# Kernel tuning notes

Measured on AMD Instinct MI355X. Metric: run time of the kernel, lower is better.

Reference implementation:

```python
import jax, jax.numpy as jnp
import numpy as np

B, T, E = 4, 2048, 2048
NH, NKV, HD = 16, 4, 128
THETA = 10000.0


def _rope(x, pos_ids, theta):
    # x: [b, h, t, hd]; pos_ids: [b, t]; theta: [hd/2]
    ang = pos_ids[:, None, :, None].astype(jnp.float32) * theta  # [b,1,t,hd/2]
    cos, sin = jnp.cos(ang), jnp.sin(ang)
    x1, x2 = x[..., ::2], x[..., 1::2]
    # interleave rotated pairs back to [..., hd]
    rot = jnp.stack([x1 * cos - x2 * sin, x1 * sin + x2 * cos], axis=-1)
    return rot.reshape(x.shape)


def setup_inputs() -> dict:
    key = jax.random.key(0)
    ks = jax.random.split(key, 10)
    s = 0.02
    x = jax.random.normal(ks[0], (B, T, E), dtype=jnp.float32)
    attention_mask = jax.random.randint(ks[1], (B, T, T), 0, 2, dtype=jnp.int32)
    # torch nn.Linear weights stored here as [in, out] (y = x @ W + b)
    Wq = jax.random.normal(ks[2], (E, E), dtype=jnp.float32) * s
    bq = jnp.zeros((E,), dtype=jnp.float32)
    Wk = jax.random.normal(ks[3], (E, NKV * HD), dtype=jnp.float32) * s
    bk = jnp.zeros((NKV * HD,), dtype=jnp.float32)
    Wv = jax.random.normal(ks[4], (E, NKV * HD), dtype=jnp.float32) * s
    bv = jnp.zeros((NKV * HD,), dtype=jnp.float32)
    Wo = jax.random.normal(ks[5], (E, E), dtype=jnp.float32) * s
    bo = jnp.zeros((E,), dtype=jnp.float32)
    return {"x": x, "attention_mask": attention_mask, "Wq": Wq, "bq": bq,
            "Wk": Wk, "bk": bk, "Wv": Wv, "bv": bv, "Wo": Wo, "bo": bo}


def reference(x, attention_mask, Wq, bq, Wk, bk, Wv, bv, Wo, bo):
    b, t = x.shape[0], x.shape[1]
    # faithful to original: plain reshape (view), NOT transpose-based head split
    q = (x @ Wq + bq).reshape(b, NH, t, HD)
    k = (x @ Wk + bk).reshape(b, NKV, t, HD)
    v = (x @ Wv + bv).reshape(b, NKV, t, HD)
    theta = THETA ** (-jnp.arange(0, HD, 2, dtype=jnp.float32) / HD)
    pos = jnp.broadcast_to(jnp.arange(t), (b, t))
    # original RoPE.forward is wrapped in @torch.no_grad() -> stop_gradient
    k = jax.lax.stop_gradient(_rope(k, pos, theta))
    v = jax.lax.stop_gradient(_rope(v, pos, theta))  # note: RoPE applied to V too
    g = NH // NKV
    k = jnp.tile(k, (1, g, 1, 1))  # torch .repeat tiles kv heads
    v = jnp.tile(v, (1, g, 1, 1))
    # original divides by head_dim ** (-0.5) == multiply by sqrt(head_dim)
    scores = jnp.einsum('bhqd,bhkd->bhqk', q, k) * (HD ** 0.5)
    scores = jnp.where(attention_mask[:, None, :, :] == 0, jnp.float32(1e-9), scores)
    attn = jax.nn.softmax(scores, axis=-1)  # dropout inactive (eval mode)
    out = jnp.einsum('bhqk,bhkd->bhqd', attn, v)
    out = out.transpose(0, 2, 1, 3).reshape(b, t, NH * HD)
    return out @ Wo + bo
```

## Files before the change

### kernel.cpp

```cpp
#include <hip/hip_runtime.h>
#include <math.h>

constexpr int Bc   = 4;
constexpr int Tc   = 2048;
constexpr int Ec   = 2048;
constexpr int NHc  = 16;
constexpr int NKVc = 4;
constexpr int HDc  = 128;
constexpr int KVEc = NKVc * HDc;

typedef __attribute__((ext_vector_type(8))) short bf16x8;
typedef __attribute__((ext_vector_type(4))) short short4v;
typedef __attribute__((ext_vector_type(4))) float f32x4;

__device__ __forceinline__ short f2bf(float f) {
    union { float f; unsigned u; } v; v.f = f;
    unsigned r = v.u + 0x7FFF + ((v.u >> 16) & 1);
    return (short)(r >> 16);
}
__device__ __forceinline__ float bf2f(short s) {
    union { unsigned u; float f; } v; v.u = ((unsigned)(unsigned short)s) << 16;
    return v.f;
}
__device__ __forceinline__ float ex2(float x) {
    float r; asm("v_exp_f32 %0, %1" : "=v"(r) : "v"(x)); return r;
}
__device__ __forceinline__ void gload16(const void* g, void* l) {
    __builtin_amdgcn_global_load_lds(
        (const __attribute__((address_space(1))) unsigned*)g,
        (__attribute__((address_space(3))) unsigned*)l, 16, 0, 0);
}

__global__ __launch_bounds__(256)
void convert_split(const float* __restrict__ X, short* __restrict__ Xhi,
                   short* __restrict__ Xlo)
{
    int i = blockIdx.x * 256 + threadIdx.x;
    float4 v = ((const float4*)X)[i];
    float fv[4] = {v.x, v.y, v.z, v.w};
    short4v hi, lo;
    #pragma unroll
    for (int j = 0; j < 4; ++j) {
        hi[j] = f2bf(fv[j]);
        lo[j] = f2bf(fv[j] - bf2f(hi[j]));
    }
    ((short4v*)Xhi)[i] = hi;
    ((short4v*)Xlo)[i] = lo;
}

__global__ __launch_bounds__(256)
void transpose_split(const float* __restrict__ W, short* __restrict__ WThi,
                     short* __restrict__ WTlo, int K, int N)
{
    __shared__ float Ls[32][33];
    const int k0 = blockIdx.x * 32, n0 = blockIdx.y * 32;
    const int t = threadIdx.x;
    const int r = t >> 3, c4 = (t & 7) << 2;
    float4 v = *(const float4*)(W + (size_t)(k0 + r) * N + n0 + c4);
    Ls[r][c4 + 0] = v.x; Ls[r][c4 + 1] = v.y;
    Ls[r][c4 + 2] = v.z; Ls[r][c4 + 3] = v.w;
    __syncthreads();
    short4v hi, lo;
    #pragma unroll
    for (int i = 0; i < 4; ++i) {
        float f = Ls[c4 + i][r];
        hi[i] = f2bf(f);
        lo[i] = f2bf(f - bf2f(hi[i]));
    }
    *(short4v*)(WThi + (size_t)(n0 + r) * K + k0 + c4) = hi;
    if (WTlo) *(short4v*)(WTlo + (size_t)(n0 + r) * K + k0 + c4) = lo;
}

__global__ __launch_bounds__(256)
void mask_bits(const int* __restrict__ mask, unsigned long long* __restrict__ Mb)
{
    const int widx = blockIdx.x * 4 + (threadIdx.x >> 6);
    const int L = threadIdx.x & 63;
    const int m = mask[(size_t)widx * 64 + L];
    unsigned long long bits = __ballot(m != 0);
    if (L == 0) Mb[widx] = bits;
}

template <bool SPLIT>
__global__ __launch_bounds__(256, 2)
void gemm_mfma(const short* __restrict__ Ahi, const short* __restrict__ Alo,
               const short* __restrict__ Bhi, const short* __restrict__ Blo,
               const float* __restrict__ bias, float* __restrict__ C,
               int M, int N, int K)
{
    __shared__ short AsH[128 * 32];
    __shared__ short BsH[128 * 32];
    __shared__ short AsL[SPLIT ? 128 * 32 : 8];
    __shared__ short BsL[SPLIT ? 128 * 32 : 8];

    const int t = threadIdx.x;
    const int w = t >> 6, L = t & 63;
    const int l16 = L & 15, quad = L >> 4;
    const int wr = w >> 1, wc = w & 1;
    const int bm = blockIdx.x * 128, bn = blockIdx.y * 128;

    const int sm = L >> 2;
    const int sq = ((L & 3) - (sm >> 2)) & 3;
    const int scol = sq * 8;

    f32x4 acc[4][4];
    #pragma unroll
    for (int mi = 0; mi < 4; ++mi)
        #pragma unroll
        for (int ni = 0; ni < 4; ++ni) acc[mi][ni] = (f32x4){0, 0, 0, 0};

    const int fxor = (quad + (l16 >> 2)) & 3;

    for (int k0 = 0; k0 < K; k0 += 32) {
        __syncthreads();
        #pragma unroll
        for (int i = 0; i < 2; ++i) {
            const int wl = w * 2 + i;
            const size_t ra = (size_t)(bm + wl * 16 + sm) * K + k0 + scol;
            const size_t rb = (size_t)(bn + wl * 16 + sm) * K + k0 + scol;
            gload16(Ahi + ra, &AsH[wl * 512]);
            gload16(Bhi + rb, &BsH[wl * 512]);
            if (SPLIT) {
                gload16(Alo + ra, &AsL[wl * 512]);
                gload16(Blo + rb, &BsL[wl * 512]);
            }
        }
        __syncthreads();

        bf16x8 ah[4], bh[4], al[4], bl[4];
        #pragma unroll
        for (int mi = 0; mi < 4; ++mi) {
            const int ch = ((wr * 4 + mi) * 64 + l16 * 4 + fxor) * 8;
            ah[mi] = *(const bf16x8*)&AsH[ch];
            if (SPLIT) al[mi] = *(const bf16x8*)&AsL[ch];
        }
        #pragma unroll
        for (int ni = 0; ni < 4; ++ni) {
            const int ch = ((wc * 4 + ni) * 64 + l16 * 4 + fxor) * 8;
            bh[ni] = *(const bf16x8*)&BsH[ch];
            if (SPLIT) bl[ni] = *(const bf16x8*)&BsL[ch];
        }
        #pragma unroll
        for (int mi = 0; mi < 4; ++mi)
            #pragma unroll
            for (int ni = 0; ni < 4; ++ni) {
                acc[mi][ni] = __builtin_amdgcn_mfma_f32_16x16x32_bf16(
                    ah[mi], bh[ni], acc[mi][ni], 0, 0, 0);
                if (SPLIT) {
                    acc[mi][ni] = __builtin_amdgcn_mfma_f32_16x16x32_bf16(
                        al[mi], bh[ni], acc[mi][ni], 0, 0, 0);
                    acc[mi][ni] = __builtin_amdgcn_mfma_f32_16x16x32_bf16(
                        ah[mi], bl[ni], acc[mi][ni], 0, 0, 0);
                }
            }
    }

    #pragma unroll
    for (int ni = 0; ni < 4; ++ni) {
        const int col = bn + wc * 64 + ni * 16 + l16;
        const float bv = bias[col];
        #pragma unroll
        for (int mi = 0; mi < 4; ++mi) {
            #pragma unroll
            for (int r = 0; r < 4; ++r) {
                const int row = bm + wr * 64 + mi * 16 + quad * 4 + r;
                C[(size_t)row * N + col] = acc[mi][ni][r] + bv;
            }
        }
    }
}

__global__ __launch_bounds__(256)
void rope_k(const float* __restrict__ X2d, short* __restrict__ Khi,
            short* __restrict__ Klo)
{
    const int idx = blockIdx.x * 256 + threadIdx.x;
    const int j  = idx & 63;
    const int tk = (idx >> 6) & (Tc - 1);
    const int kh = (idx >> 17) & (NKVc - 1);
    const int bb = idx >> 19;
    const int row = (kh << 9) + (tk >> 2);
    const int col = ((tk & 3) << 7) + (j << 1);
    const float* src = X2d + ((size_t)bb * Tc + row) * KVEc + col;
    const float a = src[0];
    const float b = src[1];
    const float theta = powf(10000.0f, -(float)j * (1.0f / 64.0f));
    const float ang = (float)tk * theta;
    float s, c;
    sincosf(ang, &s, &c);
    const float r0 = a * c - b * s;
    const float r1 = a * s + b * c;
    const size_t off = (((size_t)bb * NKVc + kh) * Tc + tk) * HDc + (j << 1);
    short h0 = f2bf(r0), h1 = f2bf(r1);
    Khi[off]     = h0;  Klo[off]     = f2bf(r0 - bf2f(h0));
    Khi[off + 1] = h1;  Klo[off + 1] = f2bf(r1 - bf2f(h1));
}

__global__ __launch_bounds__(256)
void rope_v_t(const float* __restrict__ V2d, short* __restrict__ Vt)
{
    __shared__ short Ls[128][40];
    const int g  = blockIdx.x;
    const int kh = blockIdx.y;
    const int bb = blockIdx.z;
    const int t  = threadIdx.x;

    const float* src = V2d + ((size_t)bb * Tc + (kh << 9) + (g << 3)) * KVEc;
    #pragma unroll
    for (int i = 0; i < 4; ++i) {
        int e = i * 256 + t;
        float4 v = ((const float4*)src)[e];
        int row = e >> 7;
        int col = (e & 127) << 2;
        int tkl = (row << 2) + (col >> 7);
        int d0  = col & 127;
        int tk  = (g << 5) + tkl;
        float fv[4] = {v.x, v.y, v.z, v.w};
        #pragma unroll
        for (int p = 0; p < 2; ++p) {
            int j = (d0 >> 1) + p;
            float theta = powf(10000.0f, -(float)j * (1.0f / 64.0f));
            float ang = (float)tk * theta;
            float s, c;
            sincosf(ang, &s, &c);
            float a = fv[2 * p], b = fv[2 * p + 1];
            Ls[d0 + 2 * p    ][tkl] = f2bf(a * c - b * s);
            Ls[d0 + 2 * p + 1][tkl] = f2bf(a * s + b * c);
        }
    }
    __syncthreads();
    const int d = t >> 1;
    const int h16 = (t & 1) << 4;
    short* dst = Vt + (((size_t)bb * NKVc + kh) * HDc + d) * Tc + (g << 5) + h16;
    bf16x8 o0 = *(const bf16x8*)&Ls[d][h16];
    bf16x8 o1 = *(const bf16x8*)&Ls[d][h16 + 8];
    *(bf16x8*)dst = o0;
    *(bf16x8*)(dst + 8) = o1;
}

__global__ __launch_bounds__(256, 3)
void attn_mfma(const float* __restrict__ Q2d, const short* __restrict__ Khi_g,
               const short* __restrict__ Klo_g, const short* __restrict__ Vt_g,
               const unsigned long long* __restrict__ Mb, short* __restrict__ AObf)
{
    __shared__ short KhiS[64 * 128];
    __shared__ short KloS[64 * 128];
    __shared__ short VtS [128 * 64];

    const int fid  = blockIdx.x + 32 * (blockIdx.y + 16 * blockIdx.z);
    const int slot = fid >> 3;
    const int grp  = (fid & 7) + 8 * (slot >> 5);
    const int qb   = slot & 31;
    const int h    = grp & 15;
    const int bb   = grp >> 4;

    const int t    = threadIdx.x;
    const int w    = t >> 6;
    const int L    = t & 63;
    const int l16  = L & 15;
    const int quad = L >> 4;
    const int q1v  = quad >> 1;
    const int kh   = h & (NKVc - 1);
    const int tq0  = qb * 64 + w * 16;

    bf16x8 qhi[4], qlo[4];
    {
        const float* qrow = Q2d +
            ((size_t)(bb * Tc + h * HDc + qb * 4 + w)) * Ec + 128 * l16;
        #pragma unroll
        for (int kc = 0; kc < 4; ++kc) {
            const float* p = qrow + kc * 32 + quad * 8;
            #pragma unroll
            for (int j = 0; j < 8; ++j) {
                float f = p[j];
                short hi = f2bf(f);
                qhi[kc][j] = hi;
                qlo[kc][j] = f2bf(f - bf2f(hi));
            }
        }
    }

    float m_r = -INFINITY, lp = 0.0f;
    f32x4 o[8];
    #pragma unroll
    for (int nc = 0; nc < 8; ++nc) o[nc] = (f32x4){0, 0, 0, 0};

    const short* kbh = Khi_g + ((size_t)(bb * NKVc + kh)) * Tc * HDc;
    const short* kbl = Klo_g + ((size_t)(bb * NKVc + kh)) * Tc * HDc;
    const short* vb  = Vt_g  + ((size_t)(bb * NKVc + kh)) * HDc * Tc;
    const unsigned long long* mrow =
        Mb + ((size_t)(bb * Tc + tq0 + l16)) * (Tc / 64);

    constexpr float SCALE2  = 11.313708498984761f * 1.4426950408889634f;
    constexpr float MASKED2 = 1e-9f * 1.4426950408889634f;

    const int km   = L >> 4;
    const int kpos = L & 15;
    const int vm   = L >> 3;
    const int vc   = ((L & 7) - vm) & 7;

    const int srcA = l16 + 16 * ((2 * quad)     & 3);
    const int srcB = l16 + 16 * ((2 * quad + 1) & 3);

    auto stageK = [&](int kt) {
        #pragma unroll
        for (int i = 0; i < 4; ++i) {
            const int wl = w * 4 + i;
            const int krow = wl * 4 + km;
            const int kc_ = (kpos - (krow & 15)) & 15;
            const size_t go = (size_t)(kt * 64 + krow) * HDc + kc_ * 8;
            gload16(kbh + go, &KhiS[wl * 512]);
            gload16(kbl + go, &KloS[wl * 512]);
        }
    };
    auto stageV = [&](int kt) {
        #pragma unroll
        for (int i = 0; i < 4; ++i) {
            const int wl = w * 4 + i;
            const int vrow = wl * 8 + vm;
            gload16(vb + (size_t)vrow * Tc + kt * 64 + vc * 8, &VtS[wl * 512]);
        }
    };

    asm volatile("s_waitcnt vmcnt(0)" ::: "memory");
    stageK(0);
    __builtin_amdgcn_sched_barrier(0);
    stageV(0);
    unsigned long long mw = mrow[0];

    for (int kt = 0; kt < Tc / 64; ++kt) {
        const int ktn = (kt + 1) & 31;

        asm volatile("s_waitcnt vmcnt(5)" ::: "memory");
        __builtin_amdgcn_s_barrier();
        __builtin_amdgcn_sched_barrier(0);

        f32x4 s[4];
        #pragma unroll
        for (int nt = 0; nt < 4; ++nt) {
            f32x4 acc = (f32x4){0, 0, 0, 0};
            #pragma unroll
            for (int kc = 0; kc < 4; ++kc) {
                const int ch = (((nt * 4 + (l16 >> 2)) << 6) + ((l16 & 3) << 4)
                                + ((kc * 4 + quad + l16) & 15)) << 3;
                bf16x8 khiF = *(const bf16x8*)&KhiS[ch];
                bf16x8 kloF = *(const bf16x8*)&KloS[ch];
                acc = __builtin_amdgcn_mfma_f32_16x16x32_bf16(khiF, qhi[kc], acc, 0, 0, 0);
                acc = __builtin_amdgcn_mfma_f32_16x16x32_bf16(khiF, qlo[kc], acc, 0, 0, 0);
                acc = __builtin_amdgcn_mfma_f32_16x16x32_bf16(kloF, qhi[kc], acc, 0, 0, 0);
            }
            s[nt] = acc;
        }

        asm volatile("s_waitcnt lgkmcnt(0)" ::: "memory");
        __builtin_amdgcn_sched_barrier(0);
        __builtin_amdgcn_s_barrier();
        __builtin_amdgcn_sched_barrier(0);
        stageK(ktn);
        __builtin_amdgcn_sched_barrier(0);

        const unsigned mlo = (unsigned)mw;
        const unsigned mhi = (unsigned)(mw >> 32);
        const int gq = quad << 2;
        const unsigned fm[4] = { mlo >> gq, (mlo >> 16) >> gq,
                                 mhi >> gq, (mhi >> 16) >> gq };
        #pragma unroll
        for (int nt = 0; nt < 4; ++nt)
            #pragma unroll
            for (int r = 0; r < 4; ++r)
                s[nt][r] = (fm[nt] & (1u << r)) ? s[nt][r] * SCALE2 : MASKED2;

        float mt;
        {
            float a0 = fmaxf(fmaxf(s[0][0], s[0][1]), fmaxf(s[0][2], s[0][3]));
            float a1 = fmaxf(fmaxf(s[1][0], s[1][1]), fmaxf(s[1][2], s[1][3]));
            float a2 = fmaxf(fmaxf(s[2][0], s[2][1]), fmaxf(s[2][2], s[2][3]));
            float a3 = fmaxf(fmaxf(s[3][0], s[3][1]), fmaxf(s[3][2], s[3][3]));
            mt = fmaxf(fmaxf(a0, a1), fmaxf(a2, a3));
        }
        mt = fmaxf(mt, __shfl_xor(mt, 16));
        mt = fmaxf(mt, __shfl_xor(mt, 32));

        const bool res = (mt > m_r + 8.0f);
        if (__any(res)) {
            const float mn_ = res ? mt : m_r;
            const float alq = ex2(m_r - mn_);
            m_r = mn_;
            lp *= alq;
            float alo[4];
            #pragma unroll
            for (int r = 0; r < 4; ++r)
                alo[r] = __shfl(alq, quad * 16 + quad * 4 + r);
            #pragma unroll
            for (int nc = 0; nc < 8; ++nc)
                #pragma unroll
                for (int r = 0; r < 4; ++r)
                    o[nc][r] *= alo[r];
        }

        float rs;
        {
            float t0 = 0.f, t1 = 0.f;
            #pragma unroll
            for (int nt = 0; nt < 4; ++nt) {
                float p0 = ex2(s[nt][0] - m_r);
                float p1 = ex2(s[nt][1] - m_r);
                float p2 = ex2(s[nt][2] - m_r);
                float p3 = ex2(s[nt][3] - m_r);
                s[nt][0] = p0; s[nt][1] = p1; s[nt][2] = p2; s[nt][3] = p3;
                t0 += p0 + p1; t1 += p2 + p3;
            }
            rs = t0 + t1;
        }
        lp += rs;

        int pk00, pk01, pk10, pk11, pk20, pk21, pk30, pk31;
        asm("v_cvt_pk_bf16_f32 %0, %1, %2" : "=v"(pk00) : "v"(s[0][0]), "v"(s[0][1]));
        asm("v_cvt_pk_bf16_f32 %0, %1, %2" : "=v"(pk01) : "v"(s[0][2]), "v"(s[0][3]));
        asm("v_cvt_pk_bf16_f32 %0, %1, %2" : "=v"(pk10) : "v"(s[1][0]), "v"(s[1][1]));
        asm("v_cvt_pk_bf16_f32 %0, %1, %2" : "=v"(pk11) : "v"(s[1][2]), "v"(s[1][3]));
        asm("v_cvt_pk_bf16_f32 %0, %1, %2" : "=v"(pk20) : "v"(s[2][0]), "v"(s[2][1]));
        asm("v_cvt_pk_bf16_f32 %0, %1, %2" : "=v"(pk21) : "v"(s[2][2]), "v"(s[2][3]));
        asm("v_cvt_pk_bf16_f32 %0, %1, %2" : "=v"(pk30) : "v"(s[3][0]), "v"(s[3][1]));
        asm("v_cvt_pk_bf16_f32 %0, %1, %2" : "=v"(pk31) : "v"(s[3][2]), "v"(s[3][3]));

        union U { int d[4]; bf16x8 v; } A0, A1;
        {
            int u0, u1;
            u0 = __shfl(pk00, srcA); u1 = __shfl(pk10, srcA); A0.d[0] = q1v ? u1 : u0;
            u0 = __shfl(pk01, srcA); u1 = __shfl(pk11, srcA); A0.d[1] = q1v ? u1 : u0;
            u0 = __shfl(pk00, srcB); u1 = __shfl(pk10, srcB); A0.d[2] = q1v ? u1 : u0;
            u0 = __shfl(pk01, srcB); u1 = __shfl(pk11, srcB); A0.d[3] = q1v ? u1 : u0;
            u0 = __shfl(pk20, srcA); u1 = __shfl(pk30, srcA); A1.d[0] = q1v ? u1 : u0;
            u0 = __shfl(pk21, srcA); u1 = __shfl(pk31, srcA); A1.d[1] = q1v ? u1 : u0;
            u0 = __shfl(pk20, srcB); u1 = __shfl(pk30, srcB); A1.d[2] = q1v ? u1 : u0;
            u0 = __shfl(pk21, srcB); u1 = __shfl(pk31, srcB); A1.d[3] = q1v ? u1 : u0;
        }

        asm volatile("s_waitcnt vmcnt(8)" ::: "memory");
        __builtin_amdgcn_s_barrier();
        __builtin_amdgcn_sched_barrier(0);

        #pragma unroll
        for (int nc = 0; nc < 8; ++nc) {
            const int rg = (nc * 2 + (l16 >> 3)) << 6;
            const int rm = l16 & 7;
            const int ch0 = (rg + (rm << 3) + ((quad + rm) & 7)) << 3;
            const int ch1 = (rg + (rm << 3) + ((quad + 4 + rm) & 7)) << 3;
            bf16x8 b0 = *(const bf16x8*)&VtS[ch0];
            bf16x8 b1 = *(const bf16x8*)&VtS[ch1];
            o[nc] = __builtin_amdgcn_mfma_f32_16x16x32_bf16(A0.v, b0, o[nc], 0, 0, 0);
            o[nc] = __builtin_amdgcn_mfma_f32_16x16x32_bf16(A1.v, b1, o[nc], 0, 0, 0);
        }

        asm volatile("s_waitcnt lgkmcnt(0)" ::: "memory");
        __builtin_amdgcn_sched_barrier(0);
        __builtin_amdgcn_s_barrier();
        __builtin_amdgcn_sched_barrier(0);
        stageV(ktn);
        mw = mrow[ktn];
    }

    asm volatile("s_waitcnt vmcnt(0)" ::: "memory");

    lp += __shfl_xor(lp, 16);
    lp += __shfl_xor(lp, 32);
    const float invl = 1.0f / lp;
    float invo[4];
    #pragma unroll
    for (int r = 0; r < 4; ++r)
        invo[r] = __shfl(invl, quad * 16 + quad * 4 + r);

    #pragma unroll
    for (int r = 0; r < 4; ++r) {
        short* orow = AObf + ((size_t)(bb * Tc + tq0 + quad * 4 + r)) * Ec
                           + h * HDc + l16;
        #pragma unroll
        for (int nc = 0; nc < 8; ++nc)
            orow[nc * 16] = f2bf(o[nc][r] * invo[r]);
    }
}

extern "C" void kernel_launch(void* const* d_in, const int* in_sizes, int n_in,
                              void* d_out, int out_size, void* d_ws, size_t ws_size,
                              hipStream_t stream)
{
    const float* x    = (const float*)d_in[0];
    const int*  amask = (const int*)  d_in[1];
    const float* Wq   = (const float*)d_in[2];
    const float* bq   = (const float*)d_in[3];
    const float* Wk   = (const float*)d_in[4];
    const float* bk   = (const float*)d_in[5];
    const float* Wv   = (const float*)d_in[6];
    const float* bv   = (const float*)d_in[7];
    const float* Wo   = (const float*)d_in[8];
    const float* bo   = (const float*)d_in[9];
    float* out = (float*)d_out;

    char* ws = (char*)d_ws;
    float* Q2d   = (float*)(ws);
    short* Xhi   = (short*)(ws + 67108864);
    short* Xlo   = (short*)(ws + 100663296);
    short* WqThi = (short*)(ws + 134217728);
    short* WqTlo = (short*)(ws + 134217728 + 8388608);
    float* K2d   = (float*)(ws + 150994944);
    float* V2d   = (float*)(ws + 100663296);
    short* Khi   = (short*)(ws + 100663296 + 16777216);
    short* Klo   = (short*)(ws + 100663296 + 25165824);
    short* WkThi = (short*)(ws + 134217728);
    short* WkTlo = (short*)(ws + 134217728 + 2097152);
    short* WvThi = (short*)(ws + 134217728 + 4194304);
    short* WoThi = (short*)(ws + 134217728 + 8388608);
    short* Vt    = (short*)(ws + 150994944);
    short* AObf  = (short*)(ws + 67108864);
    unsigned long long* Mb = (unsigned long long*)(ws + 167772160);

    const int M = Bc * Tc;
    dim3 blk(256);

    mask_bits<<<(Bc * Tc * (Tc / 64)) / 4, blk, 0, stream>>>(amask, Mb);
    transpose_split<<<dim3(Ec / 32, Ec / 32), blk, 0, stream>>>(Wq, WqThi, WqTlo, Ec, Ec);
    convert_split<<<(M * Ec / 4) / 256, blk, 0, stream>>>(x, Xhi, Xlo);
    gemm_mfma<true><<<dim3(M / 128, Ec / 128), blk, 0, stream>>>(
        Xhi, Xlo, WqThi, WqTlo, bq, Q2d, M, Ec, Ec);
    transpose_split<<<dim3(Ec / 32, KVEc / 32), blk, 0, stream>>>(Wk, WkThi, WkTlo, Ec, KVEc);
    transpose_split<<<dim3(Ec / 32, KVEc / 32), blk, 0, stream>>>(Wv, WvThi, nullptr, Ec, KVEc);
    transpose_split<<<dim3(Ec / 32, Ec / 32), blk, 0, stream>>>(Wo, WoThi, nullptr, Ec, Ec);
    gemm_mfma<true><<<dim3(M / 128, KVEc / 128), blk, 0, stream>>>(
        Xhi, Xlo, WkThi, WkTlo, bk, K2d, M, KVEc, Ec);
    gemm_mfma<false><<<dim3(M / 128, KVEc / 128), blk, 0, stream>>>(
        Xhi, nullptr, WvThi, nullptr, bv, V2d, M, KVEc, Ec);
    rope_k<<<(Bc * NKVc * Tc * 64) / 256, blk, 0, stream>>>(K2d, Khi, Klo);
    rope_v_t<<<dim3(Tc / 32, NKVc, Bc), blk, 0, stream>>>(V2d, Vt);
    attn_mfma<<<dim3(Tc / 64, NHc, Bc), blk, 0, stream>>>(
        Q2d, Khi, Klo, Vt, Mb, AObf);
    gemm_mfma<false><<<dim3(M / 128, Ec / 128), blk, 0, stream>>>(
        AObf, nullptr, WoThi, nullptr, bo, out, M, Ec, Ec);
}
```

Baseline: 1.059 ms.

## Process two 64-row query tiles per attention block to reuse staged K/V

Each attention workgroup now handles 128 query rows (two independent 64-row sets per wave) against the same K/V tiles staged in shared memory. This halves the K/V global-to-LDS traffic and LDS fragment reads per query, and gives more MFMA work between barriers. In exchange, register pressure roughly doubles for Q fragments and output accumulators, so launch bounds drop to 2 blocks per CU and the grid halves, which can reduce occupancy and latency hiding. The wait counts and mask loads are adjusted for the extra mask word.

```diff
diff --git a/kernel.cpp b/kernel.cpp
--- a/kernel.cpp
+++ b/kernel.cpp
@@ -238,7 +238,83 @@
     *(bf16x8*)(dst + 8) = o1;
 }
 
-__global__ __launch_bounds__(256, 3)
+#define SM_AND_P(S, MR, LPV, OACC, MW, AK0, AK1)                               \
+  do {                                                                         \
+    const unsigned mlo_ = (unsigned)(MW);                                      \
+    const unsigned mhi_ = (unsigned)((MW) >> 32);                              \
+    const int gq_ = quad << 2;                                                 \
+    const unsigned fm_0 = mlo_ >> gq_, fm_1 = (mlo_ >> 16) >> gq_;             \
+    const unsigned fm_2 = mhi_ >> gq_, fm_3 = (mhi_ >> 16) >> gq_;             \
+    _Pragma("unroll")                                                          \
+    for (int r_ = 0; r_ < 4; ++r_) {                                           \
+      S[0][r_] = (fm_0 & (1u << r_)) ? S[0][r_] * SCALE2 : MASKED2;            \
+      S[1][r_] = (fm_1 & (1u << r_)) ? S[1][r_] * SCALE2 : MASKED2;            \
+      S[2][r_] = (fm_2 & (1u << r_)) ? S[2][r_] * SCALE2 : MASKED2;            \
+      S[3][r_] = (fm_3 & (1u << r_)) ? S[3][r_] * SCALE2 : MASKED2;            \
+    }                                                                          \
+    float mt_;                                                                 \
+    {                                                                          \
+      float a0_ = fmaxf(fmaxf(S[0][0], S[0][1]), fmaxf(S[0][2], S[0][3]));     \
+      float a1_ = fmaxf(fmaxf(S[1][0], S[1][1]), fmaxf(S[1][2], S[1][3]));     \
+      float a2_ = fmaxf(fmaxf(S[2][0], S[2][1]), fmaxf(S[2][2], S[2][3]));     \
+      float a3_ = fmaxf(fmaxf(S[3][0], S[3][1]), fmaxf(S[3][2], S[3][3]));     \
+      mt_ = fmaxf(fmaxf(a0_, a1_), fmaxf(a2_, a3_));                           \
+    }                                                                          \
+    mt_ = fmaxf(mt_, __shfl_xor(mt_, 16));                                     \
+    mt_ = fmaxf(mt_, __shfl_xor(mt_, 32));                                     \
+    const bool res_ = (mt_ > (MR) + 8.0f);                                     \
+    if (__any(res_)) {                                                         \
+      const float mn_ = res_ ? mt_ : (MR);                                     \
+      const float alq_ = ex2((MR) - mn_);                                      \
+      MR = mn_;                                                                \
+      LPV *= alq_;                                                             \
+      float alo_0 = __shfl(alq_, quad * 20 + 0);                               \
+      float alo_1 = __shfl(alq_, quad * 20 + 1);                               \
+      float alo_2 = __shfl(alq_, quad * 20 + 2);                               \
+      float alo_3 = __shfl(alq_, quad * 20 + 3);                               \
+      _Pragma("unroll")                                                        \
+      for (int nc_ = 0; nc_ < 8; ++nc_) {                                      \
+        OACC[nc_][0] *= alo_0; OACC[nc_][1] *= alo_1;                          \
+        OACC[nc_][2] *= alo_2; OACC[nc_][3] *= alo_3;                          \
+      }                                                                        \
+    }                                                                          \
+    {                                                                          \
+      float t0_ = 0.f, t1_ = 0.f;                                              \
+      _Pragma("unroll")                                                        \
+      for (int nt_ = 0; nt_ < 4; ++nt_) {                                      \
+        float p0_ = ex2(S[nt_][0] - (MR));                                     \
+        float p1_ = ex2(S[nt_][1] - (MR));                                     \
+        float p2_ = ex2(S[nt_][2] - (MR));                                     \
+        float p3_ = ex2(S[nt_][3] - (MR));                                     \
+        S[nt_][0] = p0_; S[nt_][1] = p1_;                                      \
+        S[nt_][2] = p2_; S[nt_][3] = p3_;                                      \
+        t0_ += p0_ + p1_; t1_ += p2_ + p3_;                                    \
+      }                                                                        \
+      LPV += t0_ + t1_;                                                        \
+    }                                                                          \
+    int pk00_, pk01_, pk10_, pk11_, pk20_, pk21_, pk30_, pk31_;                \
+    asm("v_cvt_pk_bf16_f32 %0, %1, %2" : "=v"(pk00_) : "v"(S[0][0]), "v"(S[0][1])); \
+    asm("v_cvt_pk_bf16_f32 %0, %1, %2" : "=v"(pk01_) : "v"(S[0][2]), "v"(S[0][3])); \
+    asm("v_cvt_pk_bf16_f32 %0, %1, %2" : "=v"(pk10_) : "v"(S[1][0]), "v"(S[1][1])); \
+    asm("v_cvt_pk_bf16_f32 %0, %1, %2" : "=v"(pk11_) : "v"(S[1][2]), "v"(S[1][3])); \
+    asm("v_cvt_pk_bf16_f32 %0, %1, %2" : "=v"(pk20_) : "v"(S[2][0]), "v"(S[2][1])); \
+    asm("v_cvt_pk_bf16_f32 %0, %1, %2" : "=v"(pk21_) : "v"(S[2][2]), "v"(S[2][3])); \
+    asm("v_cvt_pk_bf16_f32 %0, %1, %2" : "=v"(pk30_) : "v"(S[3][0]), "v"(S[3][1])); \
+    asm("v_cvt_pk_bf16_f32 %0, %1, %2" : "=v"(pk31_) : "v"(S[3][2]), "v"(S[3][3])); \
+    {                                                                          \
+      int u0_, u1_;                                                            \
+      u0_ = __shfl(pk00_, srcA); u1_ = __shfl(pk10_, srcA); AK0.d[0] = q1v ? u1_ : u0_; \
+      u0_ = __shfl(pk01_, srcA); u1_ = __shfl(pk11_, srcA); AK0.d[1] = q1v ? u1_ : u0_; \
+      u0_ = __shfl(pk00_, srcB); u1_ = __shfl(pk10_, srcB); AK0.d[2] = q1v ? u1_ : u0_; \
+      u0_ = __shfl(pk01_, srcB); u1_ = __shfl(pk11_, srcB); AK0.d[3] = q1v ? u1_ : u0_; \
+      u0_ = __shfl(pk20_, srcA); u1_ = __shfl(pk30_, srcA); AK1.d[0] = q1v ? u1_ : u0_; \
+      u0_ = __shfl(pk21_, srcA); u1_ = __shfl(pk31_, srcA); AK1.d[1] = q1v ? u1_ : u0_; \
+      u0_ = __shfl(pk20_, srcB); u1_ = __shfl(pk30_, srcB); AK1.d[2] = q1v ? u1_ : u0_; \
+      u0_ = __shfl(pk21_, srcB); u1_ = __shfl(pk31_, srcB); AK1.d[3] = q1v ? u1_ : u0_; \
+    }                                                                          \
+  } while (0)
+
+__global__ __launch_bounds__(256, 2)
 void attn_mfma(const float* __restrict__ Q2d, const short* __restrict__ Khi_g,
                const short* __restrict__ Klo_g, const short* __restrict__ Vt_g,
                const unsigned long long* __restrict__ Mb, short* __restrict__ AObf)
@@ -247,10 +323,10 @@
     __shared__ short KloS[64 * 128];
     __shared__ short VtS [128 * 64];
 
-    const int fid  = blockIdx.x + 32 * (blockIdx.y + 16 * blockIdx.z);
+    const int fid  = blockIdx.x + 16 * (blockIdx.y + 16 * blockIdx.z);
     const int slot = fid >> 3;
-    const int grp  = (fid & 7) + 8 * (slot >> 5);
-    const int qb   = slot & 31;
+    const int grp  = (fid & 7) + 8 * (slot >> 4);
+    const int qb   = slot & 15;
     const int h    = grp & 15;
     const int bb   = grp >> 4;
 
@@ -261,35 +337,46 @@
     const int quad = L >> 4;
     const int q1v  = quad >> 1;
     const int kh   = h & (NKVc - 1);
-    const int tq0  = qb * 64 + w * 16;
-
-    bf16x8 qhi[4], qlo[4];
+    const int tq0  = qb * 128 + w * 16;
+    const int tq1  = tq0 + 64;
+
+    bf16x8 qhi0[4], qlo0[4], qhi1[4], qlo1[4];
     {
-        const float* qrow = Q2d +
-            ((size_t)(bb * Tc + h * HDc + qb * 4 + w)) * Ec + 128 * l16;
+        const float* qbase = Q2d +
+            ((size_t)(bb * Tc + h * HDc + qb * 8 + w)) * Ec + 128 * l16;
         #pragma unroll
         for (int kc = 0; kc < 4; ++kc) {
-            const float* p = qrow + kc * 32 + quad * 8;
+            const float* p0 = qbase + kc * 32 + quad * 8;
+            const float* p1 = p0 + (size_t)4 * Ec;
             #pragma unroll
             for (int j = 0; j < 8; ++j) {
-                float f = p[j];
-                short hi = f2bf(f);
-                qhi[kc][j] = hi;
-                qlo[kc][j] = f2bf(f - bf2f(hi));
+                float f0 = p0[j];
+                short h0 = f2bf(f0);
+                qhi0[kc][j] = h0;
+                qlo0[kc][j] = f2bf(f0 - bf2f(h0));
+                float f1 = p1[j];
+                short h1 = f2bf(f1);
+                qhi1[kc][j] = h1;
+                qlo1[kc][j] = f2bf(f1 - bf2f(h1));
             }
         }
     }
 
-    float m_r = -INFINITY, lp = 0.0f;
-    f32x4 o[8];
-    #pragma unroll
-    for (int nc = 0; nc < 8; ++nc) o[nc] = (f32x4){0, 0, 0, 0};
+    float m0 = -INFINITY, lp0 = 0.0f;
+    float m1 = -INFINITY, lp1 = 0.0f;
+    f32x4 o0[8], o1[8];
+    #pragma unroll
+    for (int nc = 0; nc < 8; ++nc) {
+        o0[nc] = (f32x4){0, 0, 0, 0};
+        o1[nc] = (f32x4){0, 0, 0, 0};
+    }
 
     const short* kbh = Khi_g + ((size_t)(bb * NKVc + kh)) * Tc * HDc;
     const short* kbl = Klo_g + ((size_t)(bb * NKVc + kh)) * Tc * HDc;
     const short* vb  = Vt_g  + ((size_t)(bb * NKVc + kh)) * HDc * Tc;
-    const unsigned long long* mrow =
+    const unsigned long long* mrow0 =
         Mb + ((size_t)(bb * Tc + tq0 + l16)) * (Tc / 64);
+    const unsigned long long* mrow1 = mrow0 + (size_t)64 * (Tc / 64);
 
     constexpr float SCALE2  = 11.313708498984761f * 1.4426950408889634f;
     constexpr float MASKED2 = 1e-9f * 1.4426950408889634f;
@@ -323,33 +410,44 @@
     };
 
     asm volatile("s_waitcnt vmcnt(0)" ::: "memory");
+    __builtin_amdgcn_sched_barrier(0);
     stageK(0);
     __builtin_amdgcn_sched_barrier(0);
     stageV(0);
-    unsigned long long mw = mrow[0];
+    __builtin_amdgcn_sched_barrier(0);
+    unsigned long long mw0 = mrow0[0];
+    unsigned long long mw1 = mrow1[0];
+    __builtin_amdgcn_sched_barrier(0);
+
+    union U { int d[4]; bf16x8 v; };
 
     for (int kt = 0; kt < Tc / 64; ++kt) {
         const int ktn = (kt + 1) & 31;
 
-        asm volatile("s_waitcnt vmcnt(5)" ::: "memory");
+        asm volatile("s_waitcnt vmcnt(6)" ::: "memory");
         __builtin_amdgcn_s_barrier();
         __builtin_amdgcn_sched_barrier(0);
 
-        f32x4 s[4];
+        f32x4 s0[4], s1[4];
         #pragma unroll
         for (int nt = 0; nt < 4; ++nt) {
-            f32x4 acc = (f32x4){0, 0, 0, 0};
+            f32x4 a0 = (f32x4){0, 0, 0, 0};
+            f32x4 a1 = (f32x4){0, 0, 0, 0};
             #pragma unroll
             for (int kc = 0; kc < 4; ++kc) {
                 const int ch = (((nt * 4 + (l16 >> 2)) << 6) + ((l16 & 3) << 4)
                                 + ((kc * 4 + quad + l16) & 15)) << 3;
                 bf16x8 khiF = *(const bf16x8*)&KhiS[ch];
                 bf16x8 kloF = *(const bf16x8*)&KloS[ch];
-                acc = __builtin_amdgcn_mfma_f32_16x16x32_bf16(khiF, qhi[kc], acc, 0, 0, 0);
-                acc = __builtin_amdgcn_mfma_f32_16x16x32_bf16(khiF, qlo[kc], acc, 0, 0, 0);
-                acc = __builtin_amdgcn_mfma_f32_16x16x32_bf16(kloF, qhi[kc], acc, 0, 0, 0);
+                a0 = __builtin_amdgcn_mfma_f32_16x16x32_bf16(khiF, qhi0[kc], a0, 0, 0, 0);
+                a0 = __builtin_amdgcn_mfma_f32_16x16x32_bf16(khiF, qlo0[kc], a0, 0, 0, 0);
+                a0 = __builtin_amdgcn_mfma_f32_16x16x32_bf16(kloF, qhi0[kc], a0, 0, 0, 0);
+                a1 = __builtin_amdgcn_mfma_f32_16x16x32_bf16(khiF, qhi1[kc], a1, 0, 0, 0);
+                a1 = __builtin_amdgcn_mfma_f32_16x16x32_bf16(khiF, qlo1[kc], a1, 0, 0, 0);
+                a1 = __builtin_amdgcn_mfma_f32_16x16x32_bf16(kloF, qhi1[kc], a1, 0, 0, 0);
             }
-            s[nt] = acc;
+            s0[nt] = a0;
+            s1[nt] = a1;
         }
 
         asm volatile("s_waitcnt lgkmcnt(0)" ::: "memory");
@@ -359,83 +457,9 @@
         stageK(ktn);
         __builtin_amdgcn_sched_barrier(0);
 
-        const unsigned mlo = (unsigned)mw;
-        const unsigned mhi = (unsigned)(mw >> 32);
-        const int gq = quad << 2;
-        const unsigned fm[4] = { mlo >> gq, (mlo >> 16) >> gq,
-                                 mhi >> gq, (mhi >> 16) >> gq };
-        #pragma unroll
-        for (int nt = 0; nt < 4; ++nt)
-            #pragma unroll
-            for (int r = 0; r < 4; ++r)
-                s[nt][r] = (fm[nt] & (1u << r)) ? s[nt][r] * SCALE2 : MASKED2;
-
-        float mt;
-        {
-            float a0 = fmaxf(fmaxf(s[0][0], s[0][1]), fmaxf(s[0][2], s[0][3]));
-            float a1 = fmaxf(fmaxf(s[1][0], s[1][1]), fmaxf(s[1][2], s[1][3]));
-            float a2 = fmaxf(fmaxf(s[2][0], s[2][1]), fmaxf(s[2][2], s[2][3]));
-            float a3 = fmaxf(fmaxf(s[3][0], s[3][1]), fmaxf(s[3][2], s[3][3]));
-            mt = fmaxf(fmaxf(a0, a1), fmaxf(a2, a3));
-        }
-        mt = fmaxf(mt, __shfl_xor(mt, 16));
-        mt = fmaxf(mt, __shfl_xor(mt, 32));
-
-        const bool res = (mt > m_r + 8.0f);
-        if (__any(res)) {
-            const float mn_ = res ? mt : m_r;
-            const float alq = ex2(m_r - mn_);
-            m_r = mn_;
-            lp *= alq;
-            float alo[4];
-            #pragma unroll
-            for (int r = 0; r < 4; ++r)
-                alo[r] = __shfl(alq, quad * 16 + quad * 4 + r);
-            #pragma unroll
-            for (int nc = 0; nc < 8; ++nc)
-                #pragma unroll
-                for (int r = 0; r < 4; ++r)
-                    o[nc][r] *= alo[r];
-        }
-
-        float rs;
-        {
-            float t0 = 0.f, t1 = 0.f;
-            #pragma unroll
-            for (int nt = 0; nt < 4; ++nt) {
-                float p0 = ex2(s[nt][0] - m_r);
-                float p1 = ex2(s[nt][1] - m_r);
-                float p2 = ex2(s[nt][2] - m_r);
-                float p3 = ex2(s[nt][3] - m_r);
-                s[nt][0] = p0; s[nt][1] = p1; s[nt][2] = p2; s[nt][3] = p3;
-                t0 += p0 + p1; t1 += p2 + p3;
-            }
-            rs = t0 + t1;
-        }
-        lp += rs;
-
-        int pk00, pk01, pk10, pk11, pk20, pk21, pk30, pk31;
-        asm("v_cvt_pk_bf16_f32 %0, %1, %2" : "=v"(pk00) : "v"(s[0][0]), "v"(s[0][1]));
-        asm("v_cvt_pk_bf16_f32 %0, %1, %2" : "=v"(pk01) : "v"(s[0][2]), "v"(s[0][3]));
-        asm("v_cvt_pk_bf16_f32 %0, %1, %2" : "=v"(pk10) : "v"(s[1][0]), "v"(s[1][1]));
-        asm("v_cvt_pk_bf16_f32 %0, %1, %2" : "=v"(pk11) : "v"(s[1][2]), "v"(s[1][3]));
-        asm("v_cvt_pk_bf16_f32 %0, %1, %2" : "=v"(pk20) : "v"(s[2][0]), "v"(s[2][1]));
-        asm("v_cvt_pk_bf16_f32 %0, %1, %2" : "=v"(pk21) : "v"(s[2][2]), "v"(s[2][3]));
-        asm("v_cvt_pk_bf16_f32 %0, %1, %2" : "=v"(pk30) : "v"(s[3][0]), "v"(s[3][1]));
-        asm("v_cvt_pk_bf16_f32 %0, %1, %2" : "=v"(pk31) : "v"(s[3][2]), "v"(s[3][3]));
-
-        union U { int d[4]; bf16x8 v; } A0, A1;
-        {
-            int u0, u1;
-            u0 = __shfl(pk00, srcA); u1 = __shfl(pk10, srcA); A0.d[0] = q1v ? u1 : u0;
-            u0 = __shfl(pk01, srcA); u1 = __shfl(pk11, srcA); A0.d[1] = q1v ? u1 : u0;
-            u0 = __shfl(pk00, srcB); u1 = __shfl(pk10, srcB); A0.d[2] = q1v ? u1 : u0;
-            u0 = __shfl(pk01, srcB); u1 = __shfl(pk11, srcB); A0.d[3] = q1v ? u1 : u0;
-            u0 = __shfl(pk20, srcA); u1 = __shfl(pk30, srcA); A1.d[0] = q1v ? u1 : u0;
-            u0 = __shfl(pk21, srcA); u1 = __shfl(pk31, srcA); A1.d[1] = q1v ? u1 : u0;
-            u0 = __shfl(pk20, srcB); u1 = __shfl(pk30, srcB); A1.d[2] = q1v ? u1 : u0;
-            u0 = __shfl(pk21, srcB); u1 = __shfl(pk31, srcB); A1.d[3] = q1v ? u1 : u0;
-        }
+        U A00, A01, A10, A11;
+        SM_AND_P(s0, m0, lp0, o0, mw0, A00, A01);
+        SM_AND_P(s1, m1, lp1, o1, mw1, A10, A11);
 
         asm volatile("s_waitcnt vmcnt(8)" ::: "memory");
         __builtin_amdgcn_s_barrier();
@@ -449,8 +473,10 @@
             const int ch1 = (rg + (rm << 3) + ((quad + 4 + rm) & 7)) << 3;
             bf16x8 b0 = *(const bf16x8*)&VtS[ch0];
             bf16x8 b1 = *(const bf16x8*)&VtS[ch1];
-            o[nc] = __builtin_amdgcn_mfma_f32_16x16x32_bf16(A0.v, b0, o[nc], 0, 0, 0);
-            o[nc] = __builtin_amdgcn_mfma_f32_16x16x32_bf16(A1.v, b1, o[nc], 0, 0, 0);
+            o0[nc] = __builtin_amdgcn_mfma_f32_16x16x32_bf16(A00.v, b0, o0[nc], 0, 0, 0);
+            o0[nc] = __builtin_amdgcn_mfma_f32_16x16x32_bf16(A01.v, b1, o0[nc], 0, 0, 0);
+            o1[nc] = __builtin_amdgcn_mfma_f32_16x16x32_bf16(A10.v, b0, o1[nc], 0, 0, 0);
+            o1[nc] = __builtin_amdgcn_mfma_f32_16x16x32_bf16(A11.v, b1, o1[nc], 0, 0, 0);
         }
 
         asm volatile("s_waitcnt lgkmcnt(0)" ::: "memory");
@@ -458,18 +484,26 @@
         __builtin_amdgcn_s_barrier();
         __builtin_amdgcn_sched_barrier(0);
         stageV(ktn);
-        mw = mrow[ktn];
+        __builtin_amdgcn_sched_barrier(0);
+        mw0 = mrow0[ktn];
+        mw1 = mrow1[ktn];
+        __builtin_amdgcn_sched_barrier(0);
     }
 
     asm volatile("s_waitcnt vmcnt(0)" ::: "memory");
 
-    lp += __shfl_xor(lp, 16);
-    lp += __shfl_xor(lp, 32);
-    const float invl = 1.0f / lp;
-    float invo[4];
-    #pragma unroll
-    for (int r = 0; r < 4; ++r)
-        invo[r] = __shfl(invl, quad * 16 + quad * 4 + r);
+    lp0 += __shfl_xor(lp0, 16);
+    lp0 += __shfl_xor(lp0, 32);
+    lp1 += __shfl_xor(lp1, 16);
+    lp1 += __shfl_xor(lp1, 32);
+    const float invl0 = 1.0f / lp0;
+    const float invl1 = 1.0f / lp1;
+    float invo0[4], invo1[4];
+    #pragma unroll
+    for (int r = 0; r < 4; ++r) {
+        invo0[r] = __shfl(invl0, quad * 16 + quad * 4 + r);
+        invo1[r] = __shfl(invl1, quad * 16 + quad * 4 + r);
+    }
 
     #pragma unroll
     for (int r = 0; r < 4; ++r) {
@@ -477,7 +511,15 @@
                            + h * HDc + l16;
         #pragma unroll
         for (int nc = 0; nc < 8; ++nc)
-            orow[nc * 16] = f2bf(o[nc][r] * invo[r]);
+            orow[nc * 16] = f2bf(o0[nc][r] * invo0[r]);
+    }
+    #pragma unroll
+    for (int r = 0; r < 4; ++r) {
+        short* orow = AObf + ((size_t)(bb * Tc + tq1 + quad * 4 + r)) * Ec
+                           + h * HDc + l16;
+        #pragma unroll
+        for (int nc = 0; nc < 8; ++nc)
+            orow[nc * 16] = f2bf(o1[nc][r] * invo1[r]);
     }
 }
 
@@ -532,7 +574,7 @@
         Xhi, nullptr, WvThi, nullptr, bv, V2d, M, KVEc, Ec);
     rope_k<<<(Bc * NKVc * Tc * 64) / 256, blk, 0, stream>>>(K2d, Khi, Klo);
     rope_v_t<<<dim3(Tc / 32, NKVc, Bc), blk, 0, stream>>>(V2d, Vt);
-    attn_mfma<<<dim3(Tc / 64, NHc, Bc), blk, 0, stream>>>(
+    attn_mfma<<<dim3(Tc / 128, NHc, Bc), blk, 0, stream>>>(
         Q2d, Khi, Klo, Vt, Mb, AObf);
     gemm_mfma<false><<<dim3(M / 128, Ec / 128), blk, 0, stream>>>(
         AObf, nullptr, WoThi, nullptr, bo, out, M, Ec, Ec);
```

Result: slower. 1.082 ms (+2.1%).
